# Kernel optimization log

Hardware: AMD Instinct MI355X
Metric: run time of the kernel (lower is better)

## Reference

```python
import jax, jax.numpy as jnp
import numpy as np

B, IN, E, H, V, T = 512, 256, 256, 512, 32000, 32


def setup_inputs() -> dict:
    key = jax.random.key(0)
    ks = jax.random.split(key, 8)
    s = 0.05
    return {
        "x": jax.random.normal(ks[0], (B, IN), jnp.float32),
        "agent_w": jax.random.normal(ks[1], (H, IN), jnp.float32) * s,
        "agent_b": jnp.zeros((H,), jnp.float32),
        "sos": jax.random.normal(ks[2], (E,), jnp.float32) * 0.01,
        "emb": jax.random.normal(ks[3], (V, E), jnp.float32) * s,
        "W_ih": jax.random.normal(ks[4], (3 * H, E), jnp.float32) * s,
        "W_hh": jax.random.normal(ks[5], (3 * H, H), jnp.float32) * s,
        "b_ih": jnp.zeros((3 * H,), jnp.float32),
        "b_hh": jnp.zeros((3 * H,), jnp.float32),
        "W_out": jax.random.normal(ks[6], (V, H), jnp.float32) * s,
        "b_out": jnp.zeros((V,), jnp.float32),
        "W_stop": jax.random.normal(ks[7], (1, H), jnp.float32) * s,
        "b_stop": jnp.zeros((1,), jnp.float32),
    }


def _gru_cell(inp, h, W_ih, W_hh, b_ih, b_hh):
    gi = inp @ W_ih.T + b_ih              # [B, 3H]
    gh = h @ W_hh.T + b_hh                # [B, 3H]
    i_r, i_z, i_n = jnp.split(gi, 3, axis=1)
    h_r, h_z, h_n = jnp.split(gh, 3, axis=1)
    r = jax.nn.sigmoid(i_r + h_r)
    z = jax.nn.sigmoid(i_z + h_z)
    n = jnp.tanh(i_n + r * h_n)
    return (1.0 - z) * n + z * h


def reference(x, agent_w, agent_b, sos, emb, W_ih, W_hh, b_ih, b_hh,
              W_out, b_out, W_stop, b_stop):
    h0 = x @ agent_w.T + agent_b                       # agent(x) -> [B, H]
    inp0 = jnp.broadcast_to(sos, (x.shape[0], sos.shape[0]))
    keys = jax.random.split(jax.random.key(42), T)

    def step(carry, k):
        h, inp = carry
        h = _gru_cell(inp, h, W_ih, W_hh, b_ih, b_hh)  # noise_scale=0 -> no noise
        symb_logits = h @ W_out.T + b_out              # [B, V]
        stop_logit = (h @ W_stop.T + b_stop)[:, 0]     # [B]
        logp = jax.nn.log_softmax(symb_logits, axis=1)
        k1, k2 = jax.random.split(k)
        symb = jax.random.categorical(k1, symb_logits, axis=1)          # [B] int
        p_stop = jax.nn.sigmoid(stop_logit)
        stop = jax.random.bernoulli(k2, p_stop).astype(jnp.float32)     # [B]
        symb_lp = jnp.take_along_axis(logp, symb[:, None], axis=1)[:, 0]
        # Bernoulli: log p = s - softplus(s), log(1-p) = -softplus(s)
        sp = jax.nn.softplus(stop_logit)
        stop_lp = stop * stop_logit - sp
        symb_ent = -jnp.sum(jnp.exp(logp) * logp, axis=1)
        stop_ent = sp - stop_logit * p_stop
        inp_next = emb[symb]
        return (h, inp_next), (symb, stop, symb_lp, stop_lp, symb_ent, stop_ent)

    _, ys = jax.lax.scan(step, (h0, inp0), keys)
    symb_seq, stop_seq, symb_lp, stop_lp, symb_ent, stop_ent = ys
    # [T, B] -> [B, T]
    tr = lambda a: a.T
    return (tr(symb_seq), tr(stop_seq).astype(jnp.int32),
            tr(symb_lp), tr(stop_lp), tr(symb_ent), tr(stop_ent))
```

## Files before the change

kernel.cpp:

```cpp
#include <hip/hip_runtime.h>
#include <hip/hip_bf16.h>
#include <stdint.h>

#define JAX_PARTITIONABLE 1

#define Bz 512
#define INz 256
#define Ez 256
#define Hz 512
#define Vz 32000
#define Tz 32
#define BTz (Bz * Tz)
#define TINYF 1.17549435e-38f

typedef float otype;
__device__ __forceinline__ void store_out(otype* out, int idx, float v) {
  out[idx] = v;
}

__device__ __forceinline__ uint32_t rotl32(uint32_t x, int r) {
  return (x << r) | (x >> (32 - r));
}
__device__ __forceinline__ void threefry2x32(uint32_t k0, uint32_t k1,
                                             uint32_t x0, uint32_t x1,
                                             uint32_t& o0, uint32_t& o1) {
  const uint32_t ks2 = k0 ^ k1 ^ 0x1BD11BDAu;
  x0 += k0; x1 += k1;
#define TF_R4(a, b, c, d)                              \
  x0 += x1; x1 = rotl32(x1, a); x1 ^= x0;              \
  x0 += x1; x1 = rotl32(x1, b); x1 ^= x0;              \
  x0 += x1; x1 = rotl32(x1, c); x1 ^= x0;              \
  x0 += x1; x1 = rotl32(x1, d); x1 ^= x0;
  TF_R4(13, 15, 26, 6)  x0 += k1;  x1 += ks2 + 1u;
  TF_R4(17, 29, 16, 24) x0 += ks2; x1 += k0 + 2u;
  TF_R4(13, 15, 26, 6)  x0 += k0;  x1 += k1 + 3u;
  TF_R4(17, 29, 16, 24) x0 += k1;  x1 += ks2 + 4u;
  TF_R4(13, 15, 26, 6)  x0 += ks2; x1 += k0 + 5u;
#undef TF_R4
  o0 = x0; o1 = x1;
}
__device__ __forceinline__ uint32_t rand_bits32(uint32_t ka, uint32_t kb,
                                                uint32_t idx, uint32_t n) {
#if JAX_PARTITIONABLE
  (void)n;
  uint32_t o0, o1;
  threefry2x32(ka, kb, 0u, idx, o0, o1);
  return o0 ^ o1;
#else
  uint32_t half = n >> 1;
  uint32_t o0, o1;
  if (idx < half) { threefry2x32(ka, kb, idx, idx + half, o0, o1); return o0; }
  threefry2x32(ka, kb, idx - half, idx, o0, o1); return o1;
#endif
}
__device__ __forceinline__ float bits_to_f01(uint32_t bits) {
  return __uint_as_float((bits >> 9) | 0x3f800000u) - 1.0f;
}

__global__ void RnnSenderReinforce_36799279792759_kernel(otype* __restrict__ out,
                                                         int n, float v) {
  int i = blockIdx.x * 256 + threadIdx.x;
  if (i < n) out[i] = v;
}

__global__ void keys_kernel(uint32_t* __restrict__ keys) {
  int t = threadIdx.x;
  if (t >= Tz) return;
  uint32_t ka, kb;
#if JAX_PARTITIONABLE
  threefry2x32(0u, 42u, 0u, (uint32_t)t, ka, kb);
#else
  {
    uint32_t j0 = 2u * t, j1 = 2u * t + 1u;
    uint32_t a0, a1, b0, b1;
    if (j0 < Tz) { threefry2x32(0u, 42u, j0, j0 + Tz, a0, a1); ka = a0; }
    else         { threefry2x32(0u, 42u, j0 - Tz, j0, a0, a1); ka = a1; }
    if (j1 < Tz) { threefry2x32(0u, 42u, j1, j1 + Tz, b0, b1); kb = b0; }
    else         { threefry2x32(0u, 42u, j1 - Tz, j1, b0, b1); kb = b1; }
  }
#endif
  uint32_t o0, o1;
#if JAX_PARTITIONABLE
  threefry2x32(ka, kb, 0u, 0u, o0, o1);
  keys[t * 4 + 0] = o0; keys[t * 4 + 1] = o1;
  threefry2x32(ka, kb, 0u, 1u, o0, o1);
  keys[t * 4 + 2] = o0; keys[t * 4 + 3] = o1;
#else
  uint32_t p0, p1, q0, q1;
  threefry2x32(ka, kb, 0u, 2u, p0, p1);
  threefry2x32(ka, kb, 1u, 3u, q0, q1);
  keys[t * 4 + 0] = p0; keys[t * 4 + 1] = q0;
  keys[t * 4 + 2] = p1; keys[t * 4 + 3] = q1;
#endif
}

#define GBM 64
#define GBN 64
#define GBK 32
#define LDSS 68

__device__ __forceinline__ void gemm_bt_body(const float* __restrict__ A,
                                             const float* __restrict__ W,
                                             const float* __restrict__ bias,
                                             float* __restrict__ C,
                                             int M, int N, int K,
                                             int bx, int by,
                                             float* As, float* Bs) {
  const int tid = threadIdx.x;
  const int tx = tid & 15;
  const int ty = tid >> 4;
  const int m0 = by * GBM;
  const int n0 = bx * GBN;
  const int lr = tid >> 3;
  const int lc = (tid & 7) << 2;

  float acc[4][4] = {};
  const float* Ap = A + (size_t)(m0 + lr) * K + lc;
  const float* Wp = W + (size_t)(n0 + lr) * K + lc;
  const size_t rstep = (size_t)32 * K;

  for (int k0 = 0; k0 < K; k0 += GBK) {
    float4 a0 = *(const float4*)(Ap + k0);
    float4 a1 = *(const float4*)(Ap + k0 + rstep);
    float4 b0 = *(const float4*)(Wp + k0);
    float4 b1 = *(const float4*)(Wp + k0 + rstep);
    __syncthreads();
    As[(lc + 0) * LDSS + lr] = a0.x;
    As[(lc + 1) * LDSS + lr] = a0.y;
    As[(lc + 2) * LDSS + lr] = a0.z;
    As[(lc + 3) * LDSS + lr] = a0.w;
    As[(lc + 0) * LDSS + lr + 32] = a1.x;
    As[(lc + 1) * LDSS + lr + 32] = a1.y;
    As[(lc + 2) * LDSS + lr + 32] = a1.z;
    As[(lc + 3) * LDSS + lr + 32] = a1.w;
    Bs[(lc + 0) * LDSS + lr] = b0.x;
    Bs[(lc + 1) * LDSS + lr] = b0.y;
    Bs[(lc + 2) * LDSS + lr] = b0.z;
    Bs[(lc + 3) * LDSS + lr] = b0.w;
    Bs[(lc + 0) * LDSS + lr + 32] = b1.x;
    Bs[(lc + 1) * LDSS + lr + 32] = b1.y;
    Bs[(lc + 2) * LDSS + lr + 32] = b1.z;
    Bs[(lc + 3) * LDSS + lr + 32] = b1.w;
    __syncthreads();
#pragma unroll
    for (int kk = 0; kk < GBK; kk++) {
      float4 af = *(const float4*)&As[kk * LDSS + (ty << 2)];
      float4 bf = *(const float4*)&Bs[kk * LDSS + (tx << 2)];
      float ar[4] = {af.x, af.y, af.z, af.w};
      float br[4] = {bf.x, bf.y, bf.z, bf.w};
#pragma unroll
      for (int i = 0; i < 4; i++)
#pragma unroll
        for (int j = 0; j < 4; j++)
          acc[i][j] = fmaf(ar[i], br[j], acc[i][j]);
    }
  }

  const int nc = n0 + (tx << 2);
  float4 bv;
  bv.x = bias[nc + 0]; bv.y = bias[nc + 1]; bv.z = bias[nc + 2]; bv.w = bias[nc + 3];
#pragma unroll
  for (int i = 0; i < 4; i++) {
    int m = m0 + (ty << 2) + i;
    float4 o;
    o.x = acc[i][0] + bv.x;
    o.y = acc[i][1] + bv.y;
    o.z = acc[i][2] + bv.z;
    o.w = acc[i][3] + bv.w;
    *(float4*)(C + (size_t)m * N + nc) = o;
  }
}

__global__ __launch_bounds__(256) void gemm_bt(const float* __restrict__ A,
                                               const float* __restrict__ W,
                                               const float* __restrict__ bias,
                                               float* __restrict__ C,
                                               int M, int N, int K) {
  __shared__ __align__(16) float As[GBK * LDSS];
  __shared__ __align__(16) float Bs[GBK * LDSS];
  gemm_bt_body(A, W, bias, C, M, N, K, blockIdx.x, blockIdx.y, As, Bs);
}

__global__ __launch_bounds__(256) void gru2_kernel(const float* __restrict__ inp,
                                                   const float* __restrict__ Wih,
                                                   const float* __restrict__ bih,
                                                   float* __restrict__ gi,
                                                   const float* __restrict__ h,
                                                   const float* __restrict__ Whh,
                                                   const float* __restrict__ bhh,
                                                   float* __restrict__ gh) {
  __shared__ __align__(16) float As[GBK * LDSS];
  __shared__ __align__(16) float Bs[GBK * LDSS];
  if (blockIdx.z == 0)
    gemm_bt_body(inp, Wih, bih, gi, Bz, 3 * Hz, Ez, blockIdx.x, blockIdx.y, As, Bs);
  else
    gemm_bt_body(h, Whh, bhh, gh, Bz, 3 * Hz, Hz, blockIdx.x, blockIdx.y, As, Bs);
}

#define QBM 256
#define QBN 128
#define QBK 32
#define QLDA 260
#define QLDB 132

__global__ __launch_bounds__(512, 4) void gemm256_bt(const float* __restrict__ A,
                                                     const float* __restrict__ W,
                                                     const float* __restrict__ bias,
                                                     float* __restrict__ C,
                                                     int M, int N, int K) {
  __shared__ __align__(16) float As[QBK * QLDA];
  __shared__ __align__(16) float Bs[QBK * QLDB];
  const int tid = threadIdx.x;
  const int tx = tid & 15;
  const int ty = tid >> 4;

  const int nP = N / QBN;
  const int G = nP >> 3;
  const int lim = G << 4;
  int b = blockIdx.x;
  int P, mi;
  if (b < lim) {
    int g = b >> 4, r = b & 15;
    mi = r >> 3;
    P = (g << 3) + (r & 7);
  } else {
    int e = b - lim;
    P = (G << 3) + (e & 1);
    mi = e >> 1;
  }
  const int m0 = mi * QBM;
  const int n0 = P * QBN;

  const int ar = tid >> 1;
  const int ak = (tid & 1) << 4;
  const int br = tid >> 2;
  const int bk = (tid & 3) << 2;

  const float* Ap = A + (size_t)(m0 + ar) * K + ak;
  const float* Wp = W + (size_t)(n0 + br) * K + bk;

  float4 a0 = *(const float4*)(Ap);
  float4 a1 = *(const float4*)(Ap + 4);
  float4 a2 = *(const float4*)(Ap + 8);
  float4 a3 = *(const float4*)(Ap + 12);
  float4 b0 = *(const float4*)(Wp);
  float4 b1 = *(const float4*)(Wp + 16);

  float acc[8][8] = {};

  for (int k0 = 0; k0 < K; k0 += QBK) {
    __syncthreads();
    As[(ak + 0) * QLDA + ar] = a0.x;
    As[(ak + 1) * QLDA + ar] = a0.y;
    As[(ak + 2) * QLDA + ar] = a0.z;
    As[(ak + 3) * QLDA + ar] = a0.w;
    As[(ak + 4) * QLDA + ar] = a1.x;
    As[(ak + 5) * QLDA + ar] = a1.y;
    As[(ak + 6) * QLDA + ar] = a1.z;
    As[(ak + 7) * QLDA + ar] = a1.w;
    As[(ak + 8) * QLDA + ar] = a2.x;
    As[(ak + 9) * QLDA + ar] = a2.y;
    As[(ak + 10) * QLDA + ar] = a2.z;
    As[(ak + 11) * QLDA + ar] = a2.w;
    As[(ak + 12) * QLDA + ar] = a3.x;
    As[(ak + 13) * QLDA + ar] = a3.y;
    As[(ak + 14) * QLDA + ar] = a3.z;
    As[(ak + 15) * QLDA + ar] = a3.w;
    Bs[(bk + 0) * QLDB + br] = b0.x;
    Bs[(bk + 1) * QLDB + br] = b0.y;
    Bs[(bk + 2) * QLDB + br] = b0.z;
    Bs[(bk + 3) * QLDB + br] = b0.w;
    Bs[(16 + bk + 0) * QLDB + br] = b1.x;
    Bs[(16 + bk + 1) * QLDB + br] = b1.y;
    Bs[(16 + bk + 2) * QLDB + br] = b1.z;
    Bs[(16 + bk + 3) * QLDB + br] = b1.w;
    __syncthreads();
    if (k0 + QBK < K) {
      a0 = *(const float4*)(Ap + k0 + QBK);
      a1 = *(const float4*)(Ap + k0 + QBK + 4);
      a2 = *(const float4*)(Ap + k0 + QBK + 8);
      a3 = *(const float4*)(Ap + k0 + QBK + 12);
      b0 = *(const float4*)(Wp + k0 + QBK);
      b1 = *(const float4*)(Wp + k0 + QBK + 16);
    }
#pragma unroll 4
    for (int kk = 0; kk < QBK; kk++) {
      float4 xa0 = *(const float4*)&As[kk * QLDA + (ty << 2)];
      float4 xa1 = *(const float4*)&As[kk * QLDA + 128 + (ty << 2)];
      float4 xb0 = *(const float4*)&Bs[kk * QLDB + (tx << 2)];
      float4 xb1 = *(const float4*)&Bs[kk * QLDB + 64 + (tx << 2)];
      float ar8[8] = {xa0.x, xa0.y, xa0.z, xa0.w, xa1.x, xa1.y, xa1.z, xa1.w};
      float br8[8] = {xb0.x, xb0.y, xb0.z, xb0.w, xb1.x, xb1.y, xb1.z, xb1.w};
#pragma unroll
      for (int i = 0; i < 8; i++)
#pragma unroll
        for (int j = 0; j < 8; j++)
          acc[i][j] = fmaf(ar8[i], br8[j], acc[i][j]);
    }
  }

  const int nc0 = n0 + (tx << 2);
  const float4 bv0 = *(const float4*)(bias + nc0);
  const float4 bv1 = *(const float4*)(bias + nc0 + 64);
#pragma unroll
  for (int hf = 0; hf < 2; hf++) {
#pragma unroll
    for (int i = 0; i < 4; i++) {
      const int m = m0 + hf * 128 + (ty << 2) + i;
      float* Cp = C + (size_t)m * N + nc0;
      float4 o;
      o.x = acc[hf * 4 + i][0] + bv0.x;
      o.y = acc[hf * 4 + i][1] + bv0.y;
      o.z = acc[hf * 4 + i][2] + bv0.z;
      o.w = acc[hf * 4 + i][3] + bv0.w;
      *(float4*)Cp = o;
      float4 o2;
      o2.x = acc[hf * 4 + i][4] + bv1.x;
      o2.y = acc[hf * 4 + i][5] + bv1.y;
      o2.z = acc[hf * 4 + i][6] + bv1.z;
      o2.w = acc[hf * 4 + i][7] + bv1.w;
      *(float4*)(Cp + 64) = o2;
    }
  }
}

__global__ __launch_bounds__(512) void gates_stop_kernel(
    const float* __restrict__ gi, const float* __restrict__ gh,
    float* __restrict__ h, const float* __restrict__ W_stop,
    const float* __restrict__ b_stop, const uint32_t* __restrict__ keys,
    int t, otype* __restrict__ out) {
  __shared__ float hrow[Hz];
  const int b = blockIdx.x;
  const int j = threadIdx.x;
  const float* gib = gi + (size_t)b * (3 * Hz);
  const float* ghb = gh + (size_t)b * (3 * Hz);
  float ir = gib[j], iz = gib[j + Hz], in_ = gib[j + 2 * Hz];
  float hr = ghb[j], hz = ghb[j + Hz], hn = ghb[j + 2 * Hz];
  float r = 1.0f / (1.0f + expf(-(ir + hr)));
  float z = 1.0f / (1.0f + expf(-(iz + hz)));
  float n = tanhf(in_ + r * hn);
  float hv = h[(size_t)b * Hz + j];
  float hnew = (1.0f - z) * n + z * hv;
  h[(size_t)b * Hz + j] = hnew;
  hrow[j] = hnew;
  __syncthreads();
  if (j < 64) {
    const int lane = j;
    float s = 0.0f;
    for (int k = lane; k < Hz; k += 64) s = fmaf(hrow[k], W_stop[k], s);
#pragma unroll
    for (int off = 32; off; off >>= 1) s += __shfl_down(s, off, 64);
    if (lane == 0) {
      s += b_stop[0];
      uint32_t bits = rand_bits32(keys[t * 4 + 2], keys[t * 4 + 3], (uint32_t)b, Bz);
      float u = bits_to_f01(bits);
      float p = 1.0f / (1.0f + expf(-s));
      float stop = (u < p) ? 1.0f : 0.0f;
      float sp = fmaxf(s, 0.0f) + log1pf(expf(-fabsf(s)));
      store_out(out, 1 * BTz + b * Tz + t, stop);
      store_out(out, 3 * BTz + b * Tz + t, stop * s - sp);
      store_out(out, 5 * BTz + b * Tz + t, sp - s * p);
    }
  }
}

__global__ __launch_bounds__(1024) void sample_p1(const float* __restrict__ logits,
                                                  const uint32_t* __restrict__ keys,
                                                  int t,
                                                  float* __restrict__ pm,
                                                  float* __restrict__ pg,
                                                  float* __restrict__ pgl,
                                                  int* __restrict__ pgi) {
  __shared__ float sm4[1024], sg4[1024], sgl4[1024];
  __shared__ int sgi4[1024];
  const int tid4 = threadIdx.x;
  const int tid = tid4 & 255;
  const int b = blockIdx.x >> 1;
  const int S = blockIdx.x & 1;
  const int sub = (S << 2) | (tid4 >> 8);
  const float* lb = logits + (size_t)b * Vz;
  const uint32_t k1a = keys[t * 4 + 0], k1b = keys[t * 4 + 1];
  const uint32_t base = (uint32_t)b * (uint32_t)Vz;

  float m = -INFINITY, gbest = -INFINITY, glogit = 0.0f;
  int gidx = 0x7FFFFFFF;
  for (int v = tid + (sub << 8); v < Vz; v += 2048) {
    float l = lb[v];
    m = fmaxf(m, l);
    uint32_t bits = rand_bits32(k1a, k1b, base + (uint32_t)v, (uint32_t)Bz * Vz);
    float f = bits_to_f01(bits);
    float u = fmaxf(TINYF, f + TINYF);
    float g = -logf(-logf(u));
    float val = l + g;
    if (val > gbest) { gbest = val; gidx = v; glogit = l; }
  }
  sm4[tid4] = m; sg4[tid4] = gbest; sgi4[tid4] = gidx; sgl4[tid4] = glogit;
  __syncthreads();
  if (tid4 < 256) {
#pragma unroll
    for (int s4 = 1; s4 < 4; s4++) {
      int o = tid4 + (s4 << 8);
      m = fmaxf(m, sm4[o]);
      float go = sg4[o]; int io = sgi4[o];
      if (go > gbest || (go == gbest && io < gidx)) {
        gbest = go; gidx = io; glogit = sgl4[o];
      }
    }
    const int o = ((b << 1) + S) * 256 + tid4;
    pm[o] = m; pg[o] = gbest; pgl[o] = glogit; pgi[o] = gidx;
  }
}

__global__ __launch_bounds__(256) void sample_p2(const float* __restrict__ logits,
                                                 const float* __restrict__ pm,
                                                 const float* __restrict__ pg,
                                                 const float* __restrict__ pgl,
                                                 const int* __restrict__ pgi,
                                                 int t, otype* __restrict__ out,
                                                 const float* __restrict__ emb,
                                                 float* __restrict__ inp) {
  __shared__ float sm[256], sg[256], sgl[256], sz[256], ss[256];
  __shared__ int sgi[256];
  __shared__ int ssymb;
  const int tid = threadIdx.x;
  const int b = blockIdx.x;
  const float* lb = logits + (size_t)b * Vz;

  const int o0 = (b << 1) * 256 + tid;
  const int o1 = o0 + 256;
  float m = fmaxf(pm[o0], pm[o1]);
  float gbest = pg[o0]; int gidx = pgi[o0]; float glogit = pgl[o0];
  {
    float go = pg[o1]; int io = pgi[o1];
    if (go > gbest || (go == gbest && io < gidx)) {
      gbest = go; gidx = io; glogit = pgl[o1];
    }
  }
  sm[tid] = m; sg[tid] = gbest; sgi[tid] = gidx; sgl[tid] = glogit;
  __syncthreads();
  for (int s2 = 128; s2; s2 >>= 1) {
    if (tid < s2) {
      sm[tid] = fmaxf(sm[tid], sm[tid + s2]);
      float go = sg[tid + s2]; int io = sgi[tid + s2];
      if (go > sg[tid] || (go == sg[tid] && io < sgi[tid])) {
        sg[tid] = go; sgi[tid] = io; sgl[tid] = sgl[tid + s2];
      }
    }
    __syncthreads();
  }
  const float M = sm[0];

  float Z = 0.0f, S1 = 0.0f;
  for (int v = tid; v < Vz; v += 256) {
    float sft = lb[v] - M;
    float e = expf(sft);
    Z += e;
    S1 = fmaf(e, sft, S1);
  }
  sz[tid] = Z; ss[tid] = S1;
  __syncthreads();
  for (int s2 = 128; s2; s2 >>= 1) {
    if (tid < s2) { sz[tid] += sz[tid + s2]; ss[tid] += ss[tid + s2]; }
    __syncthreads();
  }
  if (tid == 0) {
    float Zt = sz[0], S1t = ss[0];
    float lse = logf(Zt);
    int symb = sgi[0];
    store_out(out, 0 * BTz + b * Tz + t, (float)symb);
    store_out(out, 2 * BTz + b * Tz + t, (sgl[0] - M) - lse);
    store_out(out, 4 * BTz + b * Tz + t, lse - S1t / Zt);
    ssymb = symb;
  }
  __syncthreads();
  int s = ssymb;
  s = (s < 0) ? 0 : ((s >= Vz) ? (Vz - 1) : s);
  inp[(size_t)b * Ez + tid] = emb[(size_t)s * Ez + tid];
}

__global__ void init_inp_kernel(float* __restrict__ inp, const float* __restrict__ sos) {
  inp[blockIdx.x * Ez + threadIdx.x] = sos[threadIdx.x];
}

extern "C" __attribute__((visibility("default")))
void kernel_launch(void* const* d_in, const int* in_sizes, int n_in,
                   void* d_out, int out_size, void* d_ws, size_t ws_size,
                   hipStream_t stream) {
  const float* x       = (const float*)d_in[0];
  const float* agent_w = (const float*)d_in[1];
  const float* agent_b = (const float*)d_in[2];
  const float* sos     = (const float*)d_in[3];
  const float* emb     = (const float*)d_in[4];
  const float* W_ih    = (const float*)d_in[5];
  const float* W_hh    = (const float*)d_in[6];
  const float* b_ih    = (const float*)d_in[7];
  const float* b_hh    = (const float*)d_in[8];
  const float* W_out   = (const float*)d_in[9];
  const float* b_out   = (const float*)d_in[10];
  const float* W_stop  = (const float*)d_in[11];
  const float* b_stop  = (const float*)d_in[12];
  otype* out = (otype*)d_out;

  float* ws = (float*)d_ws;
  float* h      = ws;
  float* inp    = h + (size_t)Bz * Hz;
  float* gi     = inp + (size_t)Bz * Ez;
  float* gh     = gi + (size_t)Bz * 3 * Hz;
  float* logits = gh + (size_t)Bz * 3 * Hz;
  uint32_t* keys = (uint32_t*)(logits + (size_t)Bz * Vz);

  float* pm = gi;
  float* pg = gi + 262144;
  float* pgl = gi + 2 * 262144;
  int* pgi = (int*)gh;

  keys_kernel<<<1, 64, 0, stream>>>(keys);
  init_inp_kernel<<<Bz, Ez, 0, stream>>>(inp, sos);
  gemm_bt<<<dim3(Hz / GBN, Bz / GBM), 256, 0, stream>>>(x, agent_w, agent_b, h,
                                                        Bz, Hz, INz);
  for (int t = 0; t < Tz; t++) {
    gru2_kernel<<<dim3(3 * Hz / GBN, Bz / GBM, 2), 256, 0, stream>>>(
        inp, W_ih, b_ih, gi, h, W_hh, b_hh, gh);
    gates_stop_kernel<<<Bz, 512, 0, stream>>>(gi, gh, h, W_stop, b_stop, keys,
                                              t, out);
    gemm256_bt<<<(Vz / QBN) * (Bz / QBM), 512, 0, stream>>>(h, W_out, b_out,
                                                            logits, Bz, Vz, Hz);
    sample_p1<<<Bz * 2, 1024, 0, stream>>>(logits, keys, t, pm, pg, pgl, pgi);
    sample_p2<<<Bz, 256, 0, stream>>>(logits, pm, pg, pgl, pgi, t, out, emb,
                                      inp);
  }
}
```

Baseline: 11.12 ms.

## Fuse Gumbel-max sampling and row max into output-logits GEMM epilogue

Moves the Gumbel-noise argmax and per-row max computation from the separate sample_p1 pass into the epilogue of the vocabulary GEMM, so each tile writes per-row partial results for its 128 columns (250 partials per row). This removes one full read pass over the 512x32000 logits and one kernel launch per step. In exchange the GEMM epilogue now does the threefry RNG and log work, plus shared-memory reductions and extra barriers, which lengthens the GEMM tail and may raise register pressure.

New measurement: 11.12 ms. No clear change (+0.1%).

```diff
diff --git a/kernel.cpp b/kernel.cpp
--- a/kernel.cpp
+++ b/kernel.cpp
@@ -203,11 +203,13 @@
 #define QLDA 260
 #define QLDB 132
 
-__global__ __launch_bounds__(512, 4) void gemm256_bt(const float* __restrict__ A,
-                                                     const float* __restrict__ W,
-                                                     const float* __restrict__ bias,
-                                                     float* __restrict__ C,
-                                                     int M, int N, int K) {
+__global__ __launch_bounds__(512, 4) void gemm256_fused(
+    const float* __restrict__ A, const float* __restrict__ W,
+    const float* __restrict__ bias, float* __restrict__ C,
+    const uint32_t* __restrict__ keys, int t,
+    float* __restrict__ pv, int* __restrict__ pi,
+    float* __restrict__ pl, float* __restrict__ pmx,
+    int M, int N, int K) {
   __shared__ __align__(16) float As[QBK * QLDA];
   __shared__ __align__(16) float Bs[QBK * QLDB];
   const int tid = threadIdx.x;
@@ -302,11 +304,20 @@
   const int nc0 = n0 + (tx << 2);
   const float4 bv0 = *(const float4*)(bias + nc0);
   const float4 bv1 = *(const float4*)(bias + nc0 + 64);
+
+  __syncthreads();
+  float* vval = As;
+  int*   vidx = (int*)(As + 256 * 16);
+  float* vlgt = Bs;
+  const uint32_t k1a = keys[t * 4 + 0], k1b = keys[t * 4 + 1];
+  float pmt[8];
+
 #pragma unroll
   for (int hf = 0; hf < 2; hf++) {
 #pragma unroll
     for (int i = 0; i < 4; i++) {
-      const int m = m0 + hf * 128 + (ty << 2) + i;
+      const int r = hf * 128 + (ty << 2) + i;
+      const int m = m0 + r;
       float* Cp = C + (size_t)m * N + nc0;
       float4 o;
       o.x = acc[hf * 4 + i][0] + bv0.x;
@@ -320,7 +331,56 @@
       o2.z = acc[hf * 4 + i][6] + bv1.z;
       o2.w = acc[hf * 4 + i][7] + bv1.w;
       *(float4*)(Cp + 64) = o2;
-    }
+
+      const uint32_t base = (uint32_t)m * (uint32_t)Vz;
+      float lv[8] = {o.x, o.y, o.z, o.w, o2.x, o2.y, o2.z, o2.w};
+      float best = -INFINITY, blgt = 0.0f, mrow = -INFINITY;
+      int bidx = 0x7FFFFFFF;
+#pragma unroll
+      for (int j = 0; j < 8; j++) {
+        const int v = (j < 4) ? (nc0 + j) : (nc0 + 64 + j - 4);
+        float l = lv[j];
+        mrow = fmaxf(mrow, l);
+        uint32_t bits = rand_bits32(k1a, k1b, base + (uint32_t)v,
+                                    (uint32_t)Bz * Vz);
+        float f = bits_to_f01(bits);
+        float u = fmaxf(TINYF, f + TINYF);
+        float g = -logf(-logf(u));
+        float val = l + g;
+        if (val > best) { best = val; bidx = v; blgt = l; }
+      }
+      vval[r * 16 + tx] = best;
+      vidx[r * 16 + tx] = bidx;
+      vlgt[r * 16 + tx] = blgt;
+      pmt[hf * 4 + i] = mrow;
+    }
+  }
+  __syncthreads();
+  float rbest = 0.0f, rlgt = 0.0f;
+  int ridx = 0;
+  if (tid < 256) {
+    rbest = vval[tid * 16]; ridx = vidx[tid * 16]; rlgt = vlgt[tid * 16];
+#pragma unroll
+    for (int x = 1; x < 16; x++) {
+      float go = vval[tid * 16 + x]; int io = vidx[tid * 16 + x];
+      if (go > rbest || (go == rbest && io < ridx)) {
+        rbest = go; ridx = io; rlgt = vlgt[tid * 16 + x];
+      }
+    }
+  }
+  __syncthreads();
+#pragma unroll
+  for (int s = 0; s < 8; s++) {
+    const int r = (s >> 2) * 128 + (ty << 2) + (s & 3);
+    vval[r * 16 + tx] = pmt[s];
+  }
+  __syncthreads();
+  if (tid < 256) {
+    float mr = vval[tid * 16];
+#pragma unroll
+    for (int x = 1; x < 16; x++) mr = fmaxf(mr, vval[tid * 16 + x]);
+    const int o = (m0 + tid) * 256 + P;
+    pv[o] = rbest; pi[o] = ridx; pl[o] = rlgt; pmx[o] = mr;
   }
 }
 
@@ -364,58 +424,11 @@
   }
 }
 
-__global__ __launch_bounds__(1024) void sample_p1(const float* __restrict__ logits,
-                                                  const uint32_t* __restrict__ keys,
-                                                  int t,
-                                                  float* __restrict__ pm,
-                                                  float* __restrict__ pg,
-                                                  float* __restrict__ pgl,
-                                                  int* __restrict__ pgi) {
-  __shared__ float sm4[1024], sg4[1024], sgl4[1024];
-  __shared__ int sgi4[1024];
-  const int tid4 = threadIdx.x;
-  const int tid = tid4 & 255;
-  const int b = blockIdx.x >> 1;
-  const int S = blockIdx.x & 1;
-  const int sub = (S << 2) | (tid4 >> 8);
-  const float* lb = logits + (size_t)b * Vz;
-  const uint32_t k1a = keys[t * 4 + 0], k1b = keys[t * 4 + 1];
-  const uint32_t base = (uint32_t)b * (uint32_t)Vz;
-
-  float m = -INFINITY, gbest = -INFINITY, glogit = 0.0f;
-  int gidx = 0x7FFFFFFF;
-  for (int v = tid + (sub << 8); v < Vz; v += 2048) {
-    float l = lb[v];
-    m = fmaxf(m, l);
-    uint32_t bits = rand_bits32(k1a, k1b, base + (uint32_t)v, (uint32_t)Bz * Vz);
-    float f = bits_to_f01(bits);
-    float u = fmaxf(TINYF, f + TINYF);
-    float g = -logf(-logf(u));
-    float val = l + g;
-    if (val > gbest) { gbest = val; gidx = v; glogit = l; }
-  }
-  sm4[tid4] = m; sg4[tid4] = gbest; sgi4[tid4] = gidx; sgl4[tid4] = glogit;
-  __syncthreads();
-  if (tid4 < 256) {
-#pragma unroll
-    for (int s4 = 1; s4 < 4; s4++) {
-      int o = tid4 + (s4 << 8);
-      m = fmaxf(m, sm4[o]);
-      float go = sg4[o]; int io = sgi4[o];
-      if (go > gbest || (go == gbest && io < gidx)) {
-        gbest = go; gidx = io; glogit = sgl4[o];
-      }
-    }
-    const int o = ((b << 1) + S) * 256 + tid4;
-    pm[o] = m; pg[o] = gbest; pgl[o] = glogit; pgi[o] = gidx;
-  }
-}
-
 __global__ __launch_bounds__(256) void sample_p2(const float* __restrict__ logits,
-                                                 const float* __restrict__ pm,
-                                                 const float* __restrict__ pg,
-                                                 const float* __restrict__ pgl,
-                                                 const int* __restrict__ pgi,
+                                                 const float* __restrict__ pv,
+                                                 const int* __restrict__ pi,
+                                                 const float* __restrict__ pl,
+                                                 const float* __restrict__ pmx,
                                                  int t, otype* __restrict__ out,
                                                  const float* __restrict__ emb,
                                                  float* __restrict__ inp) {
@@ -426,15 +439,11 @@
   const int b = blockIdx.x;
   const float* lb = logits + (size_t)b * Vz;
 
-  const int o0 = (b << 1) * 256 + tid;
-  const int o1 = o0 + 256;
-  float m = fmaxf(pm[o0], pm[o1]);
-  float gbest = pg[o0]; int gidx = pgi[o0]; float glogit = pgl[o0];
-  {
-    float go = pg[o1]; int io = pgi[o1];
-    if (go > gbest || (go == gbest && io < gidx)) {
-      gbest = go; gidx = io; glogit = pgl[o1];
-    }
+  float m = -INFINITY, gbest = -INFINITY, glogit = 0.0f;
+  int gidx = 0x7FFFFFFF;
+  if (tid < 250) {
+    const int o = b * 256 + tid;
+    m = pmx[o]; gbest = pv[o]; gidx = pi[o]; glogit = pl[o];
   }
   sm[tid] = m; sg[tid] = gbest; sgi[tid] = gidx; sgl[tid] = glogit;
   __syncthreads();
@@ -509,10 +518,10 @@
   float* logits = gh + (size_t)Bz * 3 * Hz;
   uint32_t* keys = (uint32_t*)(logits + (size_t)Bz * Vz);
 
-  float* pm = gi;
-  float* pg = gi + 262144;
-  float* pgl = gi + 2 * 262144;
-  int* pgi = (int*)gh;
+  float* pv  = gi;
+  int*   pi  = (int*)(gi + 131072);
+  float* pl  = gi + 2 * 131072;
+  float* pmx = gi + 3 * 131072;
 
   keys_kernel<<<1, 64, 0, stream>>>(keys);
   init_inp_kernel<<<Bz, Ez, 0, stream>>>(inp, sos);
@@ -523,10 +532,9 @@
         inp, W_ih, b_ih, gi, h, W_hh, b_hh, gh);
     gates_stop_kernel<<<Bz, 512, 0, stream>>>(gi, gh, h, W_stop, b_stop, keys,
                                               t, out);
-    gemm256_bt<<<(Vz / QBN) * (Bz / QBM), 512, 0, stream>>>(h, W_out, b_out,
-                                                            logits, Bz, Vz, Hz);
-    sample_p1<<<Bz * 2, 1024, 0, stream>>>(logits, keys, t, pm, pg, pgl, pgi);
-    sample_p2<<<Bz, 256, 0, stream>>>(logits, pm, pg, pgl, pgi, t, out, emb,
+    gemm256_fused<<<(Vz / QBN) * (Bz / QBM), 512, 0, stream>>>(
+        h, W_out, b_out, logits, keys, t, pv, pi, pl, pmx, Bz, Vz, Hz);
+    sample_p2<<<Bz, 256, 0, stream>>>(logits, pv, pi, pl, pmx, t, out, emb,
                                       inp);
   }
 }
```
